# Kernel tuning notes

Measured on AMD Instinct MI355X. Metric: run time of the kernel, lower is better.

## Reference

```python
import jax, jax.numpy as jnp
import numpy as np

NUM_HEADS = 12


def setup_inputs() -> dict:
    key = jax.random.key(0)
    ks = jax.random.split(key, 5)
    B, S, D = 4, 2048, 768
    scale = 0.02
    return {
        "hidden_states": jax.random.normal(ks[0], (B, S, D), dtype=jnp.float32),
        "c_attn_w": jax.random.normal(ks[1], (D, 3 * D), dtype=jnp.float32) * scale,
        "c_attn_b": jax.random.normal(ks[2], (3 * D,), dtype=jnp.float32) * scale,
        "c_proj_w": jax.random.normal(ks[3], (D, D), dtype=jnp.float32) * scale,
        "c_proj_b": jax.random.normal(ks[4], (D,), dtype=jnp.float32) * scale,
    }


def reference(hidden_states, c_attn_w, c_attn_b, c_proj_w, c_proj_b):
    B, S, D = hidden_states.shape
    H = NUM_HEADS
    hd = D // H

    # fused QKV projection (HF Conv1D: x @ W + b, W is [in, out])
    qkv = hidden_states @ c_attn_w + c_attn_b  # [B, S, 3D]
    q, k, v = jnp.split(qkv, 3, axis=-1)

    def split_heads(t):
        return t.reshape(B, S, H, hd).transpose(0, 2, 1, 3)  # [B, H, S, hd]

    q, k, v = split_heads(q), split_heads(k), split_heads(v)

    # scaled dot-product scores (scale_attn_weights=True -> / sqrt(head_dim))
    scores = jnp.einsum("bhqd,bhkd->bhqk", q, k) / jnp.asarray(
        np.sqrt(hd), dtype=q.dtype
    )

    # causal mask: where(tril, scores, dtype_min) as in eager GPT2Attention
    causal = jnp.tril(jnp.ones((S, S), dtype=bool))
    mask_value = jnp.finfo(scores.dtype).min
    scores = jnp.where(causal[None, None, :, :], scores, mask_value)

    attn = jax.nn.softmax(scores, axis=-1)  # attn_dropout p=0 (eval)

    out = jnp.einsum("bhqk,bhkd->bhqd", attn, v)
    out = out.transpose(0, 2, 1, 3).reshape(B, S, D)  # merge heads

    # output projection (resid_dropout p=0)
    return out @ c_proj_w + c_proj_b
```

## Files before the change

### kernel.cpp

```cpp
#include <hip/hip_runtime.h>
#include <stdint.h>

typedef __attribute__((ext_vector_type(8))) short short8;
typedef __attribute__((ext_vector_type(4))) short short4v;
typedef __attribute__((ext_vector_type(8))) __bf16 bf16x8;
typedef __attribute__((ext_vector_type(4))) float f32x4;

#define SEQ 2048
#define DMODEL 768
#define NHEAD 12
#define HD 64
#define NBATCH 4

#define QSCALE 0.18033688011112042f

__device__ __forceinline__ float bf2f(unsigned short u) {
    return __uint_as_float(((unsigned int)u) << 16);
}
__device__ __forceinline__ unsigned short f2bf(float f) {
    unsigned int u = __float_as_uint(f);
    u += 0x7fffu + ((u >> 16) & 1u);
    return (unsigned short)(u >> 16);
}
__device__ __forceinline__ unsigned short f2bfn(float f) {
    union { __bf16 h; unsigned short u; } cv;
    cv.h = (__bf16)f;
    return cv.u;
}
__device__ __forceinline__ short8 cvt8(float4 a, float4 b) {
    short8 r;
    r[0] = (short)f2bf(a.x); r[1] = (short)f2bf(a.y);
    r[2] = (short)f2bf(a.z); r[3] = (short)f2bf(a.w);
    r[4] = (short)f2bf(b.x); r[5] = (short)f2bf(b.y);
    r[6] = (short)f2bf(b.z); r[7] = (short)f2bf(b.w);
    return r;
}
__device__ __forceinline__ f32x4 mfma16(short8 a, short8 b, f32x4 c) {
    return __builtin_amdgcn_mfma_f32_16x16x32_bf16(
        __builtin_bit_cast(bf16x8, a), __builtin_bit_cast(bf16x8, b), c, 0, 0, 0);
}
__device__ __forceinline__ f32x4 mfma16k16(short4v a, short4v b, f32x4 c) {
#if __has_builtin(__builtin_amdgcn_mfma_f32_16x16x16bf16_1k)
    return __builtin_amdgcn_mfma_f32_16x16x16bf16_1k(a, b, c, 0, 0, 0);
#else
    asm("v_mfma_f32_16x16x16_bf16 %0, %1, %2, %0" : "+v"(c) : "v"(a), "v"(b));
    return c;
#endif
}
__device__ __forceinline__ void gload16(const unsigned short* g, unsigned short* l) {
    __builtin_amdgcn_global_load_lds(
        (const __attribute__((address_space(1))) unsigned int*)g,
        (__attribute__((address_space(3))) unsigned int*)l, 16, 0, 0);
}

__global__ void detect_k(const unsigned short* x, const unsigned short* w1,
                         const unsigned short* b1, const unsigned short* w2,
                         const unsigned short* b2, int* flags) {
    const int w = threadIdx.x >> 6, l = threadIdx.x & 63;
    if (w >= 5) return;
    const unsigned short* ptrs[5] = {x, w1, b1, w2, b2};
    const unsigned short* p = ptrs[w];
    float mx = 0.f;
    for (int j = l; j < 1024; j += 64) {
        float v = fabsf(bf2f(p[j]));
        if (!(v <= 1e30f)) v = 1e31f;
        if (v > mx) mx = v;
    }
#pragma unroll
    for (int off = 1; off < 64; off <<= 1) mx = fmaxf(mx, __shfl_xor(mx, off, 64));
    if (l == 0) flags[w] = (mx > 1e3f) ? 1 : 0;
}

__global__ __launch_bounds__(256) void cvt_x(
    const float* __restrict__ Xf, const unsigned short* __restrict__ Xh,
    unsigned short* __restrict__ Xb, const int* __restrict__ flags, int n8) {
    int i = blockIdx.x * 256 + threadIdx.x;
    if (i >= n8) return;
    if (flags[0]) {
        float4 a = ((const float4*)Xf)[(size_t)i * 2];
        float4 b = ((const float4*)Xf)[(size_t)i * 2 + 1];
        *(short8*)&Xb[(size_t)i * 8] = cvt8(a, b);
    } else {
        ((uint4*)Xb)[i] = ((const uint4*)Xh)[i];
    }
}

__global__ __launch_bounds__(256) void convert_wt(
    const float* __restrict__ Wf, const unsigned short* __restrict__ Wh,
    unsigned short* __restrict__ Wt, int R, int C,
    const int* __restrict__ flags, int fidx) {

    __shared__ unsigned short tile[64][65];
    const int c0 = blockIdx.x * 64, r0 = blockIdx.y * 64;
    const int t = threadIdx.x;
    const int ri = t >> 2, cj = (t & 3) * 16;
    const bool f32 = flags[fidx] != 0;

    if (f32) {
#pragma unroll
        for (int u = 0; u < 4; u++) {
            float4 v = *(const float4*)&Wf[(size_t)(r0 + ri) * C + c0 + cj + u * 4];
            tile[ri][cj + u * 4 + 0] = f2bf(v.x);
            tile[ri][cj + u * 4 + 1] = f2bf(v.y);
            tile[ri][cj + u * 4 + 2] = f2bf(v.z);
            tile[ri][cj + u * 4 + 3] = f2bf(v.w);
        }
    } else {
        uint4 a = *(const uint4*)&Wh[(size_t)(r0 + ri) * C + c0 + cj];
        uint4 b = *(const uint4*)&Wh[(size_t)(r0 + ri) * C + c0 + cj + 8];
        *(uint4*)&tile[ri][cj] = a;
        *(uint4*)&tile[ri][cj + 8] = b;
    }
    __syncthreads();

    const int ci = t >> 2, rj = (t & 3) * 16;
    unsigned short tmp[16];
#pragma unroll
    for (int u = 0; u < 16; u++) tmp[u] = tile[rj + u][ci];
    *(uint4*)&Wt[(size_t)(c0 + ci) * R + r0 + rj]     = *(uint4*)&tmp[0];
    *(uint4*)&Wt[(size_t)(c0 + ci) * R + r0 + rj + 8] = *(uint4*)&tmp[8];
}

__global__ __launch_bounds__(256, 3) void gemm_bt(
    const float* __restrict__ Af, const unsigned short* __restrict__ Ah,
    const unsigned short* __restrict__ Bt,
    const float* __restrict__ biasf, const unsigned short* __restrict__ biash,
    int K, int mode, const int* __restrict__ flags, int aFidx, int bFidx,
    unsigned short* __restrict__ out0, unsigned short* __restrict__ out1,
    unsigned short* __restrict__ out2, float* __restrict__ outf) {

    __shared__ __align__(16) unsigned short As[2][128][32];
    __shared__ __align__(16) unsigned short Bs[2][128][32];

    int bx = blockIdx.x, by = blockIdx.y;
    {
        const int nwg = (int)(gridDim.x * gridDim.y);
        if ((nwg & 7) == 0) {
            int bid = by * gridDim.x + bx;
            const int cpx = nwg >> 3;
            bid = (bid & 7) * cpx + (bid >> 3);
            bx = bid % gridDim.x;
            by = bid / gridDim.x;
        }
    }
    const int mBase = by * 128;
    const int nBase = bx * 128;
    const int t = threadIdx.x;
    const int w = t >> 6, l = t & 63, lr = l & 15, lk = l >> 4;
    const int wr = w >> 1, wc = w & 1;

    const bool af32 = (aFidx >= 0) && (flags[aFidx] != 0);
    const bool bf32 = flags[bFidx] != 0;

    f32x4 zero = {0.f, 0.f, 0.f, 0.f};
    f32x4 acc[4][4];
#pragma unroll
    for (int i = 0; i < 4; i++)
#pragma unroll
        for (int j = 0; j < 4; j++) acc[i][j] = zero;

    const int arow2 = t >> 1;
    const int ha32 = t & 1;
    const float* Afp = Af + (size_t)mBase * K;
    const unsigned short* Ahp = Ah + (size_t)mBase * K;
    const unsigned short* Bp = Bt + (size_t)nBase * K;

    unsigned short* BsF = &Bs[0][0][0];
    unsigned short* AsF = &As[0][0][0];

    for (int k0 = 0; k0 < K; k0 += 64) {
#pragma unroll
        for (int q = 0; q < 4; q++) {
            const int c = q * 256 + t;
            const int row = (c >> 2) & 127;
            const int ha = c >> 9;
            const int g2 = c & 3;
            gload16(&Bp[(size_t)row * K + k0 + ha * 32 + g2 * 8],
                    BsF + (size_t)(q * 256 + w * 64) * 8);
        }
        if (af32) {
#pragma unroll
            for (int u = 0; u < 4; u++) {
                float4 f0 = *(const float4*)&Afp[(size_t)arow2 * K + k0 + ha32 * 32 + u * 8];
                float4 f1 = *(const float4*)&Afp[(size_t)arow2 * K + k0 + ha32 * 32 + u * 8 + 4];
                *(short8*)&As[ha32][arow2][u * 8] = cvt8(f0, f1);
            }
        } else {
#pragma unroll
            for (int q = 0; q < 4; q++) {
                const int c = q * 256 + t;
                const int row = (c >> 2) & 127;
                const int ha = c >> 9;
                const int g2 = c & 3;
                gload16(&Ahp[(size_t)row * K + k0 + ha * 32 + g2 * 8],
                        AsF + (size_t)(q * 256 + w * 64) * 8);
            }
        }
        __syncthreads();

#pragma unroll
        for (int ha = 0; ha < 2; ha++) {
            short8 a[4], b[4];
#pragma unroll
            for (int i = 0; i < 4; i++)
                a[i] = *(const short8*)&As[ha][wr * 64 + i * 16 + lr][lk * 8];
#pragma unroll
            for (int j = 0; j < 4; j++)
                b[j] = *(const short8*)&Bs[ha][wc * 64 + j * 16 + lr][lk * 8];
#pragma unroll
            for (int i = 0; i < 4; i++)
#pragma unroll
                for (int j = 0; j < 4; j++) acc[i][j] = mfma16(a[i], b[j], acc[i][j]);
        }
        __syncthreads();
    }

#pragma unroll
    for (int j = 0; j < 4; j++) {
        int col = nBase + wc * 64 + j * 16 + lr;
        float bv = bf32 ? biasf[col] : bf2f(biash[col]);
        if (mode == 0 && col >= 1536) {
            int c2 = col - 1536;
            int h = c2 >> 6, d = c2 & 63;
#pragma unroll
            for (int i = 0; i < 4; i++) {
                int row0 = mBase + wr * 64 + i * 16 + lk * 4;
                int bb = row0 >> 11, s0 = row0 & 2047;
                short4v hv4;
#pragma unroll
                for (int r = 0; r < 4; r++) hv4[r] = (short)f2bf(acc[i][j][r] + bv);
                *(short4v*)&out2[(((size_t)(bb * NHEAD + h)) * HD + d) * SEQ + s0] = hv4;
            }
        } else {
#pragma unroll
            for (int i = 0; i < 4; i++) {
                int row0 = mBase + wr * 64 + i * 16 + lk * 4;
#pragma unroll
                for (int r = 0; r < 4; r++) {
                    int row = row0 + r;
                    float fv = acc[i][j][r] + bv;
                    if (mode == 0) {
                        int bb = row >> 11;
                        int s  = row & 2047;
                        if (col < 768) {
                            int h = col >> 6, d = col & 63;
                            out0[(((size_t)(bb * NHEAD + h)) * SEQ + s) * HD + d] =
                                f2bf(fv * QSCALE);
                        } else {
                            int c2 = col - 768;
                            int h = c2 >> 6, d = c2 & 63;
                            out1[(((size_t)(bb * NHEAD + h)) * SEQ + s) * HD + d] =
                                f2bf(fv);
                        }
                    } else {
                        outf[(size_t)row * DMODEL + col] = fv;
                    }
                }
            }
        }
    }
}

__global__ __launch_bounds__(256, 3) void flash_attn(
    const unsigned short* __restrict__ Q, const unsigned short* __restrict__ Km,
    const unsigned short* __restrict__ Vt, unsigned short* __restrict__ Oatt) {

    const int h  = blockIdx.x;
    const int px = blockIdx.y;
    const int b  = blockIdx.z;
    const int bh = b * NHEAD + h;
    const int qtA = 31 - px;
    const int qtB = px;
    const int t = threadIdx.x, w = t >> 6, l = t & 63, lr = l & 15, lk = l >> 4;
    const int qbA = qtA * 64 + w * 16;
    const int qbB = qtB * 64 + w * 16;

    const unsigned short* Qp = Q + (size_t)bh * SEQ * HD;
    const unsigned short* Kp = Km + (size_t)bh * SEQ * HD;
    const unsigned short* Vp = Vt + (size_t)bh * HD * SEQ;

    __shared__ __align__(16) unsigned short Ks[2][4096];
    __shared__ __align__(16) unsigned short Vs[2][4096];

    short8 qA0 = *(const short8*)&Qp[(size_t)(qbA + lr) * HD + lk * 8];
    short8 qA1 = *(const short8*)&Qp[(size_t)(qbA + lr) * HD + 32 + lk * 8];
    short8 qB0 = *(const short8*)&Qp[(size_t)(qbB + lr) * HD + lk * 8];
    short8 qB1 = *(const short8*)&Qp[(size_t)(qbB + lr) * HD + 32 + lk * 8];

    f32x4 zero = {0.f, 0.f, 0.f, 0.f};
    f32x4 oA[4], oB[4];
    float lsumA = 0.f, lsumB = 0.f;
#pragma unroll
    for (int dt = 0; dt < 4; dt++) { oA[dt] = zero; oB[dt] = zero; }

#pragma unroll
    for (int q = 0; q < 2; ++q) {
        const int c = w * 128 + q * 64 + l;
        const int row = c >> 3;
        const int ch = (c & 7) ^ (row & 7);
        gload16(&Kp[(size_t)row * HD + ch * 8], &Ks[0][(w * 128 + q * 64) * 8]);
        gload16(&Vp[(size_t)row * SEQ + ch * 8], &Vs[0][(w * 128 + q * 64) * 8]);
    }
    __syncthreads();

    for (int kt = 0; kt <= qtA; ++kt) {
        const int cur = kt & 1;
        if (kt < qtA) {
            const int kn = kt + 1;
#pragma unroll
            for (int q = 0; q < 2; ++q) {
                const int c = w * 128 + q * 64 + l;
                const int row = c >> 3;
                const int ch = (c & 7) ^ (row & 7);
                gload16(&Kp[(size_t)(kn * 64 + row) * HD + ch * 8],
                        &Ks[cur ^ 1][(w * 128 + q * 64) * 8]);
                gload16(&Vp[(size_t)row * SEQ + kn * 64 + ch * 8],
                        &Vs[cur ^ 1][(w * 128 + q * 64) * 8]);
            }
        }
        const bool doB = (kt <= qtB);

        f32x4 s0[4], s1[4];
#pragma unroll
        for (int ct = 0; ct < 4; ct++) { s0[ct] = zero; s1[ct] = zero; }
#pragma unroll
        for (int ct = 0; ct < 4; ct++) {
            const int row = ct * 16 + lr, sw = row & 7;
            short8 k0 = *(const short8*)&Ks[cur][(row * 8 + (lk ^ sw)) * 8];
            short8 k1 = *(const short8*)&Ks[cur][(row * 8 + ((4 | lk) ^ sw)) * 8];
            s0[ct] = mfma16(k0, qA0, s0[ct]);
            s0[ct] = mfma16(k1, qA1, s0[ct]);
            if (doB) {
                s1[ct] = mfma16(k0, qB0, s1[ct]);
                s1[ct] = mfma16(k1, qB1, s1[ct]);
            }
        }

        short4v vf[4][4];
#pragma unroll
        for (int dt = 0; dt < 4; dt++) {
            const int row = dt * 16 + lr;
            const int sw = row & 7;
#pragma unroll
            for (int ct = 0; ct < 4; ct++) {
                const int g = 2 * ct + (lk >> 1);
                const int hh = lk & 1;
                vf[dt][ct] = *(const short4v*)&Vs[cur][(row * 8 + (g ^ sw)) * 8 + hh * 4];
            }
        }

        short4v paA[4];
        {
            float p[4][4];
#pragma unroll
            for (int ct = 0; ct < 4; ct++)
#pragma unroll
                for (int r = 0; r < 4; r++) p[ct][r] = exp2f(s0[ct][r]);
            if (kt == qtA) {
                const int qrow = qbA + lr;
#pragma unroll
                for (int ct = 0; ct < 4; ct++)
#pragma unroll
                    for (int r = 0; r < 4; r++) {
                        const int key = kt * 64 + ct * 16 + lk * 4 + r;
                        if (key > qrow) p[ct][r] = 0.0f;
                    }
            }
#pragma unroll
            for (int ct = 0; ct < 4; ct++)
                lsumA += (p[ct][0] + p[ct][1]) + (p[ct][2] + p[ct][3]);
#pragma unroll
            for (int ct = 0; ct < 4; ct++) {
                short4v pk;
#pragma unroll
                for (int r = 0; r < 4; r++) pk[r] = (short)f2bfn(p[ct][r]);
                paA[ct] = pk;
            }
        }
#pragma unroll
        for (int dt = 0; dt < 4; dt++)
#pragma unroll
            for (int ct = 0; ct < 4; ct++)
                oA[dt] = mfma16k16(paA[ct], vf[dt][ct], oA[dt]);

        if (doB) {
            short4v paB[4];
            float p[4][4];
#pragma unroll
            for (int ct = 0; ct < 4; ct++)
#pragma unroll
                for (int r = 0; r < 4; r++) p[ct][r] = exp2f(s1[ct][r]);
            if (kt == qtB) {
                const int qrow = qbB + lr;
#pragma unroll
                for (int ct = 0; ct < 4; ct++)
#pragma unroll
                    for (int r = 0; r < 4; r++) {
                        const int key = kt * 64 + ct * 16 + lk * 4 + r;
                        if (key > qrow) p[ct][r] = 0.0f;
                    }
            }
#pragma unroll
            for (int ct = 0; ct < 4; ct++)
                lsumB += (p[ct][0] + p[ct][1]) + (p[ct][2] + p[ct][3]);
#pragma unroll
            for (int ct = 0; ct < 4; ct++) {
                short4v pk;
#pragma unroll
                for (int r = 0; r < 4; r++) pk[r] = (short)f2bfn(p[ct][r]);
                paB[ct] = pk;
            }
#pragma unroll
            for (int dt = 0; dt < 4; dt++)
#pragma unroll
                for (int ct = 0; ct < 4; ct++)
                    oB[dt] = mfma16k16(paB[ct], vf[dt][ct], oB[dt]);
        }

        __syncthreads();
    }

    lsumA += __shfl_xor(lsumA, 16, 64);
    lsumA += __shfl_xor(lsumA, 32, 64);
    lsumB += __shfl_xor(lsumB, 16, 64);
    lsumB += __shfl_xor(lsumB, 32, 64);

#pragma unroll
    for (int r = 0; r < 4; r++) {
        const float invA = 1.0f / __shfl(lsumA, lk * 4 + r, 64);
        const float invB = 1.0f / __shfl(lsumB, lk * 4 + r, 64);
        const int rowA = qbA + lk * 4 + r;
        const int rowB = qbB + lk * 4 + r;
#pragma unroll
        for (int dt = 0; dt < 4; dt++) {
            Oatt[((size_t)(b * SEQ) + rowA) * DMODEL + h * HD + dt * 16 + lr] =
                f2bfn(oA[dt][r] * invA);
            Oatt[((size_t)(b * SEQ) + rowB) * DMODEL + h * HD + dt * 16 + lr] =
                f2bfn(oB[dt][r] * invB);
        }
    }
}

extern "C" void kernel_launch(void* const* d_in, const int* in_sizes, int n_in,
                              void* d_out, int out_size, void* d_ws, size_t ws_size,
                              hipStream_t stream) {
    const void *X = d_in[0], *W1 = d_in[1], *b1 = d_in[2], *W2 = d_in[3], *b2 = d_in[4];
    for (int i = 0; i < n_in; i++) {
        switch (in_sizes[i]) {
            case NBATCH * SEQ * DMODEL: X  = d_in[i]; break;
            case DMODEL * 3 * DMODEL:   W1 = d_in[i]; break;
            case 3 * DMODEL:            b1 = d_in[i]; break;
            case DMODEL * DMODEL:       W2 = d_in[i]; break;
            case DMODEL:                b2 = d_in[i]; break;
        }
    }
    float* out = (float*)d_out;

    int* flags = (int*)d_ws;
    unsigned short* base = (unsigned short*)d_ws + 64;
    unsigned short* Wt1 = base;
    unsigned short* Wt2 = Wt1 + (size_t)2304 * 768;

    const size_t headElems = (size_t)NHEAD * SEQ * HD;
    const size_t xElems = (size_t)NBATCH * SEQ * DMODEL;
    const size_t fixedElems = 64 + (size_t)2304 * 768 + (size_t)768 * 768;
    const size_t mergedNeed = (fixedElems + xElems + 4 * NBATCH * headElems) * 2 + 1024;
    const bool merged = ws_size >= mergedNeed;

    detect_k<<<1, 320, 0, stream>>>(
        (const unsigned short*)X, (const unsigned short*)W1,
        (const unsigned short*)b1, (const unsigned short*)W2,
        (const unsigned short*)b2, flags);

    convert_wt<<<dim3(2304 / 64, 768 / 64), 256, 0, stream>>>(
        (const float*)W1, (const unsigned short*)W1, Wt1, 768, 2304, flags, 1);
    convert_wt<<<dim3(768 / 64, 768 / 64), 256, 0, stream>>>(
        (const float*)W2, (const unsigned short*)W2, Wt2, 768, 768, flags, 3);

    if (merged) {
        unsigned short* Xb  = Wt2 + (size_t)768 * 768;
        unsigned short* Qw  = Xb + xElems;
        unsigned short* Kw  = Qw + (size_t)NBATCH * headElems;
        unsigned short* Vtw = Kw + (size_t)NBATCH * headElems;
        unsigned short* Aw  = Vtw + (size_t)NBATCH * headElems;

        cvt_x<<<(int)((xElems / 8 + 255) / 256), 256, 0, stream>>>(
            (const float*)X, (const unsigned short*)X, Xb, flags, (int)(xElems / 8));

        gemm_bt<<<dim3(2304 / 128, NBATCH * SEQ / 128), 256, 0, stream>>>(
            nullptr, Xb, Wt1,
            (const float*)b1, (const unsigned short*)b1,
            DMODEL, 0, flags, -1, 2, Qw, Kw, Vtw, nullptr);

        flash_attn<<<dim3(NHEAD, 16, NBATCH), 256, 0, stream>>>(Qw, Kw, Vtw, Aw);

        gemm_bt<<<dim3(768 / 128, NBATCH * SEQ / 128), 256, 0, stream>>>(
            nullptr, Aw, Wt2,
            (const float*)b2, (const unsigned short*)b2,
            DMODEL, 1, flags, -1, 4, nullptr, nullptr, nullptr, out);
    } else {
        unsigned short* Qw  = Wt2 + (size_t)768 * 768;
        unsigned short* Kw  = Qw + headElems;
        unsigned short* Vtw = Kw + headElems;
        unsigned short* Aw  = Vtw + headElems;
        for (int batch = 0; batch < NBATCH; ++batch) {
            const size_t xoff = (size_t)batch * SEQ * DMODEL;

            gemm_bt<<<dim3(2304 / 128, SEQ / 128), 256, 0, stream>>>(
                (const float*)X + xoff, (const unsigned short*)X + xoff, Wt1,
                (const float*)b1, (const unsigned short*)b1,
                DMODEL, 0, flags, 0, 2, Qw, Kw, Vtw, nullptr);

            flash_attn<<<dim3(NHEAD, 16, 1), 256, 0, stream>>>(Qw, Kw, Vtw, Aw);

            gemm_bt<<<dim3(768 / 128, SEQ / 128), 256, 0, stream>>>(
                nullptr, Aw, Wt2,
                (const float*)b2, (const unsigned short*)b2,
                DMODEL, 1, flags, -1, 4, nullptr, nullptr, nullptr, out + xoff);
        }
    }
}
```

Baseline: 225.2 us.

## Triple-buffer K/V tiles in flash attention with two-ahead prefetch

Switches the K/V shared-memory staging from double to triple buffering, prefetching tile kt+2 while computing tile kt. Full __syncthreads is replaced by explicit vmcnt waits that leave the newest tile's loads in flight, followed by a raw s_barrier. This aims to hide more global-load latency, at the cost of 50% more LDS per block (48KB), which may cut occupancy below the 3 blocks/CU the launch bounds request.

```diff
diff --git a/kernel.cpp b/kernel.cpp
--- a/kernel.cpp
+++ b/kernel.cpp
@@ -261,6 +261,19 @@
     }
 }
 
+#define STAGE(buf, tile) do {                                                  \
+    _Pragma("unroll")                                                          \
+    for (int q_ = 0; q_ < 2; ++q_) {                                           \
+        const int c_ = w * 128 + q_ * 64 + l;                                  \
+        const int row_ = c_ >> 3;                                              \
+        const int ch_ = (c_ & 7) ^ (row_ & 7);                                 \
+        gload16(&Kp[(size_t)((tile) * 64 + row_) * HD + ch_ * 8],              \
+                &Ks[buf][(w * 128 + q_ * 64) * 8]);                            \
+        gload16(&Vp[(size_t)row_ * SEQ + (tile) * 64 + ch_ * 8],               \
+                &Vs[buf][(w * 128 + q_ * 64) * 8]);                            \
+    }                                                                          \
+} while (0)
+
 __global__ __launch_bounds__(256, 3) void flash_attn(
     const unsigned short* __restrict__ Q, const unsigned short* __restrict__ Km,
     const unsigned short* __restrict__ Vt, unsigned short* __restrict__ Oatt) {
@@ -279,8 +292,8 @@
     const unsigned short* Kp = Km + (size_t)bh * SEQ * HD;
     const unsigned short* Vp = Vt + (size_t)bh * HD * SEQ;
 
-    __shared__ __align__(16) unsigned short Ks[2][4096];
-    __shared__ __align__(16) unsigned short Vs[2][4096];
+    __shared__ __align__(16) unsigned short Ks[3][4096];
+    __shared__ __align__(16) unsigned short Vs[3][4096];
 
     short8 qA0 = *(const short8*)&Qp[(size_t)(qbA + lr) * HD + lk * 8];
     short8 qA1 = *(const short8*)&Qp[(size_t)(qbA + lr) * HD + 32 + lk * 8];
@@ -293,30 +306,17 @@
 #pragma unroll
     for (int dt = 0; dt < 4; dt++) { oA[dt] = zero; oB[dt] = zero; }
 
-#pragma unroll
-    for (int q = 0; q < 2; ++q) {
-        const int c = w * 128 + q * 64 + l;
-        const int row = c >> 3;
-        const int ch = (c & 7) ^ (row & 7);
-        gload16(&Kp[(size_t)row * HD + ch * 8], &Ks[0][(w * 128 + q * 64) * 8]);
-        gload16(&Vp[(size_t)row * SEQ + ch * 8], &Vs[0][(w * 128 + q * 64) * 8]);
-    }
-    __syncthreads();
-
+    STAGE(0, 0);
+    STAGE(1, 1);
+    asm volatile("s_waitcnt vmcnt(4)" ::: "memory");
+    __builtin_amdgcn_s_barrier();
+
+    int cur = 0;
     for (int kt = 0; kt <= qtA; ++kt) {
-        const int cur = kt & 1;
-        if (kt < qtA) {
-            const int kn = kt + 1;
-#pragma unroll
-            for (int q = 0; q < 2; ++q) {
-                const int c = w * 128 + q * 64 + l;
-                const int row = c >> 3;
-                const int ch = (c & 7) ^ (row & 7);
-                gload16(&Kp[(size_t)(kn * 64 + row) * HD + ch * 8],
-                        &Ks[cur ^ 1][(w * 128 + q * 64) * 8]);
-                gload16(&Vp[(size_t)row * SEQ + kn * 64 + ch * 8],
-                        &Vs[cur ^ 1][(w * 128 + q * 64) * 8]);
-            }
+        const bool pf = (kt + 2 <= qtA);
+        if (pf) {
+            const int st = (cur == 0) ? 2 : cur - 1;
+            STAGE(st, kt + 2);
         }
         const bool doB = (kt <= qtB);
 
@@ -417,7 +417,12 @@
                     oB[dt] = mfma16k16(paB[ct], vf[dt][ct], oB[dt]);
         }
 
-        __syncthreads();
+        if (kt < qtA) {
+            if (pf) asm volatile("s_waitcnt vmcnt(4)" ::: "memory");
+            else    asm volatile("s_waitcnt vmcnt(0)" ::: "memory");
+            __builtin_amdgcn_s_barrier();
+        }
+        cur = (cur == 2) ? 0 : cur + 1;
     }
 
     lsumA += __shfl_xor(lsumA, 16, 64);
```

New measurement: 226.0 us. No clear change (+0.4%).
